# Kernel optimization log

Measured on AMD Instinct MI355X. Metric: run time of the kernel, lower is better.

Reference implementation:

```python
import jax, jax.numpy as jnp
import numpy as np

B, R, C_M, C_Z, H, DH, NQP = 2, 384, 384, 128, 12, 32, 4
W_C = (2.0 / (9 * NQP)) ** (-0.5)   # (2/(9*n_qp))^-0.5
W_L = 3.0 ** 0.5                     # (1/3)^-0.5


def setup_inputs() -> dict:
    key = jax.random.key(0)
    ks = jax.random.split(key, 10)
    pair_rep = jax.random.normal(ks[0], (B, R, R, C_Z), jnp.float32)
    sing_rep = jax.random.normal(ks[1], (B, R, C_M), jnp.float32)
    m = jax.random.normal(ks[2], (B, R, 3, 3), jnp.float32)
    bbr, _ = jnp.linalg.qr(m)  # orthonormal backbone frames (B,R,3,3)
    bbt = jax.random.normal(ks[3], (B, R, 3), jnp.float32)
    s = 0.02
    W_qkv = jax.random.normal(ks[4], (C_M, DH * 3 * H), jnp.float32) * s
    W_qk = jax.random.normal(ks[5], (C_M, H * 2 * NQP * 3), jnp.float32) * s
    W_fc1 = jax.random.normal(ks[6], (C_Z, H), jnp.float32) * s
    b_fc1 = jnp.zeros((H,), jnp.float32)
    W0 = jax.random.normal(ks[7], (H * DH, C_M), jnp.float32) * s
    W1 = jax.random.normal(ks[8], (H * C_Z, C_M), jnp.float32) * s
    gamma = jax.random.uniform(ks[9], (1,), jnp.float32)
    return dict(pair_rep=pair_rep, sing_rep=sing_rep, bbr=bbr, bbt=bbt,
                W_qkv=W_qkv, W_qk=W_qk, W_fc1=W_fc1, b_fc1=b_fc1,
                W0=W0, W1=W1, gamma=gamma)


def reference(pair_rep, sing_rep, bbr, bbt, W_qkv, W_qk, W_fc1, b_fc1, W0, W1, gamma):
    # pair bias: fc1 then b i j h -> b h i j
    pair_bias = jnp.transpose(jnp.einsum('bijc,ch->bijh', pair_rep, W_fc1) + b_fc1,
                              (0, 3, 1, 2))                      # b h i j
    # scalar q/k/v: channel layout (dim_head, 3, heads)
    qkv = (sing_rep @ W_qkv).reshape(B, R, DH, 3, H)
    rq, rk, rv = (jnp.transpose(qkv[:, :, :, i, :], (0, 3, 1, 2)) for i in range(3))  # b h r d
    dot = jnp.einsum('bhid,bhjd->bhij', rq, rk) * DH ** (-0.5)
    # point q/k: channel layout (heads, 2, n_qp, 3)
    qk = (sing_rep @ W_qk).reshape(B, R, H, 2, NQP, 3)
    gq = jnp.transpose(qk[:, :, :, 0], (0, 3, 1, 2, 4))          # b p r h a
    gk = jnp.transpose(qk[:, :, :, 1], (0, 3, 1, 2, 4))
    # frame-transformed query/key points
    Tq = jnp.einsum('bprha,brak->phbrk', gq, bbr) + bbt          # p h b r 3
    Tk = jnp.einsum('bprha,brak->phbrk', gk, bbr) + bbt
    diff = Tq[:, :, :, :, None, :] - Tk[:, :, :, None, :, :]     # p h b i j 3
    sq = jnp.transpose(jnp.sum(diff * diff, axis=(0, -1)), (1, 0, 2, 3))  # b h i j
    head_w = jax.nn.softplus(gamma[0]) * W_C / 2                 # same scalar per head
    attn = jax.nn.softmax(W_L * (pair_bias + dot + head_w * sq), axis=-1)
    # pair-rep value aggregation -> W_1
    top = jnp.einsum('bhij,bijc->bihc', attn, pair_rep).reshape(B, R, H * C_Z) @ W1
    # scalar value aggregation -> W_0   (note: original adds these two only;
    # the point-value 'bot' branch is computed but unused in the output)
    out = jnp.transpose(jnp.einsum('bhij,bhjd->bhid', attn, rv),
                        (0, 2, 1, 3)).reshape(B, R, H * DH) @ W0
    return out + top
```

## Files before the change

### kernel.cpp

```cpp
#include <hip/hip_runtime.h>
#include <math.h>

#define Bb   2
#define Rr   384
#define CMd  384
#define CZ   128
#define Hh   12
#define DHd  32

#define WL           1.7320508075688772f
#define WC           4.242640687119285f
#define INV_SQRT_DH  0.17677669529663687f

#define SZ_R   (Bb*Hh*Rr*DHd)
#define SZ_T   (Bb*Hh*Rr*12)
#define SZ_S   (Bb*Hh*Rr)
#define SZ_A   ((long)Bb*Hh*Rr*Rr)
#define SZ_O   (Bb*Rr*Hh*DHd)

__global__ __launch_bounds__(64) void k_projgemm(
    const float* __restrict__ sing, const float* __restrict__ Wqkv,
    const float* __restrict__ Wqk, float* __restrict__ pbuf)
{
  const int t = threadIdx.x;
  const int m0 = blockIdx.x * 32;
  const int n0 = blockIdx.y * 32;
  const int ks = blockIdx.z;
  const int tx = t & 7, ty = t >> 3;
  __shared__ float As[32][36];
  __shared__ float Bs[32][36];
  float acc[4][4] = {};

  for (int kc = ks*192; kc < ks*192 + 192; kc += 32) {
    #pragma unroll
    for (int i = 0; i < 4; ++i) {
      int s = t + 64*i;
      int row = s >> 3, k4 = (s & 7) << 2;
      float4 v = *(const float4*)(sing + (long)(m0 + row)*384 + kc + k4);
      As[k4  ][row] = v.x; As[k4+1][row] = v.y;
      As[k4+2][row] = v.z; As[k4+3][row] = v.w;
    }
    #pragma unroll
    for (int i = 0; i < 4; ++i) {
      int s = t + 64*i;
      int k = s >> 3, c4 = (s & 7) << 2;
      const float* srcB = (n0 < 1152)
          ? Wqkv + (long)(kc + k)*1152 + n0 + c4
          : Wqk  + (long)(kc + k)*288 + (n0 - 1152) + c4;
      float4 w = *(const float4*)srcB;
      Bs[k][c4] = w.x; Bs[k][c4+1] = w.y; Bs[k][c4+2] = w.z; Bs[k][c4+3] = w.w;
    }
    __syncthreads();
    #pragma unroll
    for (int k = 0; k < 32; ++k) {
      float4 a = *(const float4*)&As[k][ty*4];
      float4 b = *(const float4*)&Bs[k][tx*4];
      acc[0][0] += a.x*b.x; acc[0][1] += a.x*b.y; acc[0][2] += a.x*b.z; acc[0][3] += a.x*b.w;
      acc[1][0] += a.y*b.x; acc[1][1] += a.y*b.y; acc[1][2] += a.y*b.z; acc[1][3] += a.y*b.w;
      acc[2][0] += a.z*b.x; acc[2][1] += a.z*b.y; acc[2][2] += a.z*b.z; acc[2][3] += a.z*b.w;
      acc[3][0] += a.w*b.x; acc[3][1] += a.w*b.y; acc[3][2] += a.w*b.z; acc[3][3] += a.w*b.w;
    }
    __syncthreads();
  }
  float* pd = pbuf + (long)ks * (768*1440);
  #pragma unroll
  for (int i = 0; i < 4; ++i)
    *(float4*)&pd[(long)(m0 + ty*4 + i)*1440 + n0 + tx*4] =
        make_float4(acc[i][0], acc[i][1], acc[i][2], acc[i][3]);
}

__global__ __launch_bounds__(256) void k_scatter(
    const float* __restrict__ pbuf,
    float* __restrict__ rq, float* __restrict__ rk, float* __restrict__ rv,
    float* __restrict__ gbuf)
{
  const int idx = blockIdx.x*256 + threadIdx.x;
  const int row = idx / 360;
  const int n   = (idx - row*360) * 4;
  float4 a = ((const float4*)pbuf)[idx];
  float4 b = ((const float4*)(pbuf + (long)768*1440))[idx];
  float v[4] = {a.x + b.x, a.y + b.y, a.z + b.z, a.w + b.w};
  const int bb = row / Rr, rr = row - bb*Rr;
  #pragma unroll
  for (int j = 0; j < 4; ++j) {
    int nj = n + j;
    if (nj < 1152) {
      int d = nj/36, rem = nj - d*36, wh = rem/12, h = rem - wh*12;
      float* dst = (wh == 0) ? rq : (wh == 1) ? rk : rv;
      dst[(((long)bb*Hh + h)*Rr + rr)*DHd + d] = v[j];
    } else {
      gbuf[(long)row*288 + nj - 1152] = v[j];
    }
  }
}

__global__ __launch_bounds__(256) void k_frame(
    const float* __restrict__ gbuf, const float* __restrict__ bbr,
    const float* __restrict__ bbt,
    float* __restrict__ TqF, float* __restrict__ TkF,
    float* __restrict__ Qsq, float* __restrict__ Ksq)
{
  const int idx = blockIdx.x*256 + threadIdx.x;
  const int row = idx / 24, q = idx - row*24;
  const int h = q >> 1, s2 = q & 1;
  const float* gp = gbuf + (long)row*288 + h*24 + s2*12;
  float rot[9], tr[3];
  #pragma unroll
  for (int a = 0; a < 9; ++a) rot[a] = bbr[(long)row*9 + a];
  #pragma unroll
  for (int a = 0; a < 3; ++a) tr[a] = bbt[(long)row*3 + a];
  const int b = row / Rr, r = row - b*Rr;
  float* T = s2 ? TkF : TqF;
  const long tb = (((long)b*Hh + h)*Rr + r)*12;
  float v[12]; float ss = 0.f;
  #pragma unroll
  for (int p = 0; p < 4; ++p)
    #pragma unroll
    for (int k2 = 0; k2 < 3; ++k2) {
      float x = gp[p*3+0]*rot[k2] + gp[p*3+1]*rot[3+k2] + gp[p*3+2]*rot[6+k2] + tr[k2];
      v[p*3+k2] = x; ss += x*x;
    }
  *(float4*)(T + tb)     = make_float4(v[0], v[1], v[2],  v[3]);
  *(float4*)(T + tb + 4) = make_float4(v[4], v[5], v[6],  v[7]);
  *(float4*)(T + tb + 8) = make_float4(v[8], v[9], v[10], v[11]);
  (s2 ? Ksq : Qsq)[((long)b*Hh + h)*Rr + r] = ss;
}

__global__ __launch_bounds__(256) void k_pbias(
    const float* __restrict__ pair, const float* __restrict__ Wfc1,
    const float* __restrict__ bfc1, float* __restrict__ pb)
{
  const int t = threadIdx.x;
  const long base = (long)blockIdx.x * 64;
  __shared__ float tile[64][129];
  __shared__ float w_l[128][12];
  __shared__ float bias_l[12];
  for (int idx = t; idx < 128*12; idx += 256) w_l[idx/12][idx%12] = Wfc1[idx];
  if (t < 12) bias_l[t] = bfc1[t];
  const float4* src = (const float4*)(pair + base*CZ);
  for (int idx = t; idx < 64*32; idx += 256) {
    float4 v = src[idx];
    int row = idx >> 5, c4 = (idx & 31) << 2;
    tile[row][c4] = v.x; tile[row][c4+1] = v.y; tile[row][c4+2] = v.z; tile[row][c4+3] = v.w;
  }
  __syncthreads();
  int row = t & 63;
  long n = base + row;
  int b = (int)(n / ((long)Rr*Rr));
  long rr2 = n - (long)b*Rr*Rr;
  int i = (int)(rr2 / Rr), j = (int)(rr2 - (long)i*Rr);
  int h0 = t >> 6;
  float a0 = bias_l[h0], a1 = bias_l[h0+4], a2 = bias_l[h0+8];
  for (int c = 0; c < 128; ++c) {
    float v = tile[row][c];
    a0 += v*w_l[c][h0]; a1 += v*w_l[c][h0+4]; a2 += v*w_l[c][h0+8];
  }
  long o = (((long)b*Hh + h0)*Rr + i)*Rr + j;
  const long hstride = (long)Rr*Rr*4;
  pb[o] = a0; pb[o + hstride] = a1; pb[o + 2*hstride] = a2;
}

#define ITILE 8
__global__ __launch_bounds__(256) void k_scores(
    const float* __restrict__ rq, const float* __restrict__ rk,
    const float* __restrict__ TqF, const float* __restrict__ TkF,
    const float* __restrict__ Qsq, const float* __restrict__ Ksq,
    const float* __restrict__ gamma, float* __restrict__ attn)
{
  const int t = threadIdx.x;
  const int nt = Rr / ITILE;
  const int bh = blockIdx.x / nt;
  const int i0 = (blockIdx.x - bh*nt) * ITILE;
  __shared__ float rk_l[384][33];
  __shared__ float rq_l[32];
  __shared__ float tq_l[12];
  __shared__ float scal[1];
  __shared__ float redm[4], reds[4];

  for (int idx = t; idx < 384*32; idx += 256)
    rk_l[idx >> 5][idx & 31] = rk[(long)bh*Rr*DHd + idx];

  const float g0 = gamma[0];
  const float head_w = log1pf(__expf(g0)) * (WC * 0.5f);

  for (int ii = 0; ii < ITILE; ++ii) {
    const int i = i0 + ii;
    if (t < 32) rq_l[t] = rq[((long)bh*Rr + i)*DHd + t];
    if (t < 12) tq_l[t] = TqF[((long)bh*Rr + i)*12 + t];
    if (t == 0) scal[0] = Qsq[(long)bh*Rr + i];
    __syncthreads();
    const float qs = scal[0];
    const long rowbase = ((long)bh*Rr + i)*Rr;

    auto logit_at = [&](int j) -> float {
      float dt = 0.f;
      #pragma unroll
      for (int dd = 0; dd < 32; ++dd) dt += rq_l[dd] * rk_l[j][dd];
      const float4* tk = (const float4*)(TkF + ((long)bh*Rr + j)*12);
      float4 ta = tk[0], tb = tk[1], tc = tk[2];
      float pt = tq_l[0]*ta.x + tq_l[1]*ta.y + tq_l[2]*ta.z + tq_l[3]*ta.w
               + tq_l[4]*tb.x + tq_l[5]*tb.y + tq_l[6]*tb.z + tq_l[7]*tb.w
               + tq_l[8]*tc.x + tq_l[9]*tc.y + tq_l[10]*tc.z + tq_l[11]*tc.w;
      float sqv = qs + Ksq[(long)bh*Rr + j] - 2.f*pt;
      return WL * (attn[rowbase + j] + dt*INV_SQRT_DH + head_w*sqv);
    };

    float l0 = logit_at(t);
    float l1 = (t < 128) ? logit_at(t + 256) : -3.4e38f;
    float m = fmaxf(l0, l1);
    #pragma unroll
    for (int s = 32; s; s >>= 1) m = fmaxf(m, __shfl_xor(m, s, 64));
    if ((t & 63) == 0) redm[t >> 6] = m;
    __syncthreads();
    m = fmaxf(fmaxf(redm[0], redm[1]), fmaxf(redm[2], redm[3]));
    float e0 = __expf(l0 - m);
    float e1 = (t < 128) ? __expf(l1 - m) : 0.f;
    float s = e0 + e1;
    #pragma unroll
    for (int sh = 32; sh; sh >>= 1) s += __shfl_xor(s, sh, 64);
    if ((t & 63) == 0) reds[t >> 6] = s;
    __syncthreads();
    float inv = 1.f / (reds[0] + reds[1] + reds[2] + reds[3]);
    attn[rowbase + t] = e0 * inv;
    if (t < 128) attn[rowbase + t + 256] = e1 * inv;
    __syncthreads();
  }
}

__global__ __launch_bounds__(256) void k_agg(
    const float* __restrict__ attn, const float* __restrict__ pair,
    const float* __restrict__ rv, float* __restrict__ o_ihd, float* __restrict__ top)
{
  const int t = threadIdx.x;
  const int bi = blockIdx.x;
  const int b = bi / Rr;
  const int i = bi - b*Rr;
  __shared__ float a_l[12][384];
  for (int idx = t; idx < 12*384; idx += 256) {
    int h = idx / 384, j = idx - h*384;
    a_l[h][j] = attn[(((long)b*Hh + h)*Rr + i)*Rr + j];
  }
  __syncthreads();
  const int c = t & 127, hh = t >> 7;
  const float* prow = pair + (long)bi * Rr * CZ;
  float acc0=0,acc1=0,acc2=0,acc3=0,acc4=0,acc5=0;
  for (int j = 0; j < 384; ++j) {
    float v = prow[(long)j*CZ + c];
    acc0 += a_l[hh   ][j]*v;
    acc1 += a_l[hh+2 ][j]*v;
    acc2 += a_l[hh+4 ][j]*v;
    acc3 += a_l[hh+6 ][j]*v;
    acc4 += a_l[hh+8 ][j]*v;
    acc5 += a_l[hh+10][j]*v;
  }
  float* tp = top + ((long)bi*Hh)*CZ + c;
  tp[(long)(hh   )*CZ] = acc0;
  tp[(long)(hh+2 )*CZ] = acc1;
  tp[(long)(hh+4 )*CZ] = acc2;
  tp[(long)(hh+6 )*CZ] = acc3;
  tp[(long)(hh+8 )*CZ] = acc4;
  tp[(long)(hh+10)*CZ] = acc5;
  for (int o = t; o < 384; o += 256) {
    int h = o >> 5, dd = o & 31;
    const float* rvp = rv + ((long)b*Hh + h)*Rr*DHd + dd;
    float s = 0.f;
    for (int j = 0; j < 384; ++j) s += a_l[h][j] * rvp[(long)j*DHd];
    o_ihd[(long)bi*384 + o] = s;
  }
}

#define K5_KSPLIT 6
#define K5_KLEN   320
__global__ __launch_bounds__(64) void k_final_part(
    const float* __restrict__ o_ihd, const float* __restrict__ top,
    const float* __restrict__ W0, const float* __restrict__ W1,
    float* __restrict__ partial)
{
  const int t = threadIdx.x;
  const int m0 = blockIdx.x * 32;
  const int n0 = blockIdx.y * 32;
  const int ks = blockIdx.z;
  const int tx = t & 7, ty = t >> 3;
  __shared__ float As[32][36];
  __shared__ float Bs[32][36];
  float acc[4][4] = {};

  for (int kc = ks*K5_KLEN; kc < ks*K5_KLEN + K5_KLEN; kc += 32) {
    #pragma unroll
    for (int i = 0; i < 4; ++i) {
      int s = t + 64*i;
      int row = s >> 3, k4 = (s & 7) << 2;
      int gk = kc + k4;
      const float* srcA = (gk < 384)
          ? o_ihd + (long)(m0 + row)*384 + gk
          : top   + (long)(m0 + row)*1536 + (gk - 384);
      float4 v = *(const float4*)srcA;
      As[k4  ][row] = v.x; As[k4+1][row] = v.y;
      As[k4+2][row] = v.z; As[k4+3][row] = v.w;
    }
    #pragma unroll
    for (int i = 0; i < 4; ++i) {
      int s = t + 64*i;
      int k = s >> 3, c4 = (s & 7) << 2;
      int gk = kc + k;
      const float* srcB = (gk < 384)
          ? W0 + (long)gk*384 + n0 + c4
          : W1 + (long)(gk - 384)*384 + n0 + c4;
      float4 w = *(const float4*)srcB;
      Bs[k][c4] = w.x; Bs[k][c4+1] = w.y; Bs[k][c4+2] = w.z; Bs[k][c4+3] = w.w;
    }
    __syncthreads();
    #pragma unroll
    for (int k = 0; k < 32; ++k) {
      float4 a = *(const float4*)&As[k][ty*4];
      float4 b = *(const float4*)&Bs[k][tx*4];
      acc[0][0] += a.x*b.x; acc[0][1] += a.x*b.y; acc[0][2] += a.x*b.z; acc[0][3] += a.x*b.w;
      acc[1][0] += a.y*b.x; acc[1][1] += a.y*b.y; acc[1][2] += a.y*b.z; acc[1][3] += a.y*b.w;
      acc[2][0] += a.z*b.x; acc[2][1] += a.z*b.y; acc[2][2] += a.z*b.z; acc[2][3] += a.z*b.w;
      acc[3][0] += a.w*b.x; acc[3][1] += a.w*b.y; acc[3][2] += a.w*b.z; acc[3][3] += a.w*b.w;
    }
    __syncthreads();
  }
  float* pdst = partial + (long)ks * (768*384);
  #pragma unroll
  for (int i = 0; i < 4; ++i)
    *(float4*)&pdst[(long)(m0 + ty*4 + i)*384 + n0 + tx*4] =
        make_float4(acc[i][0], acc[i][1], acc[i][2], acc[i][3]);
}

__global__ __launch_bounds__(256) void k_final_reduce(
    const float* __restrict__ partial, float* __restrict__ out)
{
  const int idx = blockIdx.x*256 + threadIdx.x;
  float4 r = make_float4(0.f, 0.f, 0.f, 0.f);
  #pragma unroll
  for (int p = 0; p < K5_KSPLIT; ++p) {
    float4 a = ((const float4*)(partial + (long)p*768*384))[idx];
    r.x += a.x; r.y += a.y; r.z += a.z; r.w += a.w;
  }
  ((float4*)out)[idx] = r;
}

extern "C" void kernel_launch(void* const* d_in, const int* in_sizes, int n_in,
                              void* d_out, int out_size, void* d_ws, size_t ws_size,
                              hipStream_t stream)
{
  (void)in_sizes; (void)n_in; (void)out_size; (void)ws_size;
  const float* pair  = (const float*)d_in[0];
  const float* sing  = (const float*)d_in[1];
  const float* bbr   = (const float*)d_in[2];
  const float* bbt   = (const float*)d_in[3];
  const float* Wqkv  = (const float*)d_in[4];
  const float* Wqk   = (const float*)d_in[5];
  const float* Wfc1  = (const float*)d_in[6];
  const float* bfc1  = (const float*)d_in[7];
  const float* W0    = (const float*)d_in[8];
  const float* W1    = (const float*)d_in[9];
  const float* gamma = (const float*)d_in[10];
  float* out = (float*)d_out;

  float* ws    = (float*)d_ws;
  float* rq    = ws;
  float* rk    = rq  + SZ_R;
  float* rv    = rk  + SZ_R;
  float* TqF   = rv  + SZ_R;
  float* TkF   = TqF + SZ_T;
  float* Qsq   = TkF + SZ_T;
  float* Ksq   = Qsq + SZ_S;
  float* attn  = Ksq + SZ_S;
  float* o_ihd = attn + SZ_A;
  float* top   = o_ihd + SZ_O;
  float* gbuf  = o_ihd;
  float* pbuf  = attn;
  float* partial = attn;

  k_projgemm<<<dim3(24, 45, 2), dim3(64), 0, stream>>>(sing, Wqkv, Wqk, pbuf);
  k_scatter<<<dim3(276480/256), dim3(256), 0, stream>>>(pbuf, rq, rk, rv, gbuf);
  k_frame<<<dim3(Bb*Rr*24/256), dim3(256), 0, stream>>>(
      gbuf, bbr, bbt, TqF, TkF, Qsq, Ksq);
  k_pbias<<<dim3(Bb*Rr*Rr/64), dim3(256), 0, stream>>>(pair, Wfc1, bfc1, attn);
  k_scores<<<dim3(Bb*Hh*(Rr/ITILE)), dim3(256), 0, stream>>>(
      rq, rk, TqF, TkF, Qsq, Ksq, gamma, attn);
  k_agg<<<dim3(Bb*Rr), dim3(256), 0, stream>>>(attn, pair, rv, o_ihd, top);
  k_final_part<<<dim3(24, 12, K5_KSPLIT), dim3(64), 0, stream>>>(
      o_ihd, top, W0, W1, partial);
  k_final_reduce<<<dim3(768*384/4/256), dim3(256), 0, stream>>>(partial, out);
}
```

Measured before the change: 205.9 us.

## Restructure pair-bias kernel to one row per thread with register accumulation

```diff
diff --git a/kernel.cpp b/kernel.cpp
--- a/kernel.cpp
+++ b/kernel.cpp
@@ -131,33 +131,32 @@
     const float* __restrict__ bfc1, float* __restrict__ pb)
 {
   const int t = threadIdx.x;
-  const long base = (long)blockIdx.x * 64;
-  __shared__ float tile[64][129];
-  __shared__ float w_l[128][12];
+  __shared__ __align__(16) float w_t[12*128];
   __shared__ float bias_l[12];
-  for (int idx = t; idx < 128*12; idx += 256) w_l[idx/12][idx%12] = Wfc1[idx];
+  for (int s = t; s < 1536; s += 256) {
+    int h = s >> 7, c = s & 127;
+    w_t[s] = Wfc1[c*12 + h];
+  }
   if (t < 12) bias_l[t] = bfc1[t];
-  const float4* src = (const float4*)(pair + base*CZ);
-  for (int idx = t; idx < 64*32; idx += 256) {
-    float4 v = src[idx];
-    int row = idx >> 5, c4 = (idx & 31) << 2;
-    tile[row][c4] = v.x; tile[row][c4+1] = v.y; tile[row][c4+2] = v.z; tile[row][c4+3] = v.w;
-  }
   __syncthreads();
-  int row = t & 63;
-  long n = base + row;
-  int b = (int)(n / ((long)Rr*Rr));
-  long rr2 = n - (long)b*Rr*Rr;
-  int i = (int)(rr2 / Rr), j = (int)(rr2 - (long)i*Rr);
-  int h0 = t >> 6;
-  float a0 = bias_l[h0], a1 = bias_l[h0+4], a2 = bias_l[h0+8];
-  for (int c = 0; c < 128; ++c) {
-    float v = tile[row][c];
-    a0 += v*w_l[c][h0]; a1 += v*w_l[c][h0+4]; a2 += v*w_l[c][h0+8];
-  }
-  long o = (((long)b*Hh + h0)*Rr + i)*Rr + j;
-  const long hstride = (long)Rr*Rr*4;
-  pb[o] = a0; pb[o + hstride] = a1; pb[o + 2*hstride] = a2;
+
+  const long r0 = (long)blockIdx.x*256 + t;
+  const float4* pr0 = (const float4*)pair + r0*32;
+  float acc0[12] = {};
+  #pragma unroll 4
+  for (int cc = 0; cc < 32; ++cc) {
+    float4 p0 = pr0[cc];
+    #pragma unroll
+    for (int h = 0; h < 12; ++h) {
+      float4 wv = *(const float4*)&w_t[h*128 + cc*4];
+      acc0[h] += p0.x*wv.x + p0.y*wv.y + p0.z*wv.z + p0.w*wv.w;
+    }
+  }
+  int b0 = (int)(r0 / 147456); long rm = r0 - (long)b0*147456;
+  int i0 = (int)(rm / 384), j0 = (int)(rm - i0*384);
+  #pragma unroll
+  for (int h = 0; h < 12; ++h)
+    pb[(((long)b0*Hh + h)*Rr + i0)*Rr + j0] = acc0[h] + bias_l[h];
 }
 
 #define ITILE 8
@@ -378,7 +377,7 @@
   k_scatter<<<dim3(276480/256), dim3(256), 0, stream>>>(pbuf, rq, rk, rv, gbuf);
   k_frame<<<dim3(Bb*Rr*24/256), dim3(256), 0, stream>>>(
       gbuf, bbr, bbt, TqF, TkF, Qsq, Ksq);
-  k_pbias<<<dim3(Bb*Rr*Rr/64), dim3(256), 0, stream>>>(pair, Wfc1, bfc1, attn);
+  k_pbias<<<dim3(1152), dim3(256), 0, stream>>>(pair, Wfc1, bfc1, attn);
   k_scores<<<dim3(Bb*Hh*(Rr/ITILE)), dim3(256), 0, stream>>>(
       rq, rk, TqF, TkF, Qsq, Ksq, gamma, attn);
   k_agg<<<dim3(Bb*Rr), dim3(256), 0, stream>>>(attn, pair, rv, o_ihd, top);
```

New measurement: 198.3 us. -3.7%, faster.
